# Optimization experiments

Hardware: AMD Instinct MI355X
Metric: run time of the kernel (lower is better)

## Reference

```python
import jax, jax.numpy as jnp
import numpy as np

N_NODES = 50000
N_EDGES = 400000
IN_DIM = 256
EPS_BN = 1e-5


def _bn(x, gamma, beta):
    # BatchNorm over nodes (training-mode batch statistics)
    m = jnp.mean(x, axis=0)
    v = jnp.var(x, axis=0)
    return (x - m) * jax.lax.rsqrt(v + EPS_BN) * gamma + beta


def _gcn(x, W, b, src, dst, n):
    # PyG GCNConv: add self-loops, symmetric deg^-1/2 normalization
    h = x @ W  # [N, F_out]
    deg = jax.ops.segment_sum(jnp.ones_like(dst, dtype=h.dtype), dst, num_segments=n) + 1.0
    dinv = jax.lax.rsqrt(deg)
    coef = dinv[src] * dinv[dst]  # [E]
    agg = jax.ops.segment_sum(h[src] * coef[:, None], dst, num_segments=n)
    agg = agg + h * (dinv * dinv)[:, None]  # self-loop contribution
    return agg + b


def _gat(x, W, a_src, a_dst, b, src, dst, n):
    # PyG GATConv, heads=H, concat=False (mean over heads)
    H, F = a_src.shape
    h = (x @ W).reshape(n, H, F)
    asc = jnp.einsum('nhf,hf->nh', h, a_src)
    adc = jnp.einsum('nhf,hf->nh', h, a_dst)
    loops = jnp.arange(n, dtype=src.dtype)
    s = jnp.concatenate([src, loops])
    d = jnp.concatenate([dst, loops])
    e = jax.nn.leaky_relu(asc[s] + adc[d], 0.2)  # [E+N, H]
    mx = jax.ops.segment_max(e, d, num_segments=n)
    ee = jnp.exp(e - mx[d])
    denom = jax.ops.segment_sum(ee, d, num_segments=n)
    alpha = ee / (denom[d] + 1e-16)  # edge softmax over incoming edges
    out = jax.ops.segment_sum(alpha[:, :, None] * h[s], d, num_segments=n)  # [N,H,F]
    return out.mean(axis=1) + b


def setup_inputs() -> dict:
    key = jax.random.key(0)
    ks = jax.random.split(key, 24)

    def glorot(k, shape):
        fan = shape[0] + shape[-1]
        return jax.random.normal(k, shape, jnp.float32) * np.sqrt(2.0 / fan)

    d = {}
    d['x'] = jax.random.normal(ks[0], (N_NODES, IN_DIM), jnp.float32)
    d['edge_index'] = jax.random.randint(ks[1], (2, N_EDGES), 0, N_NODES, jnp.int32)
    # GCNConv 1: 256 -> 256
    d['w1'] = glorot(ks[2], (IN_DIM, 256)); d['b1'] = jnp.zeros((256,), jnp.float32)
    d['g1'] = jnp.ones((256,), jnp.float32); d['be1'] = jnp.zeros((256,), jnp.float32)
    # GATConv: 256 -> 128, heads=4, concat=False
    d['gat_w'] = glorot(ks[3], (256, 4 * 128))
    d['gat_as'] = glorot(ks[4], (4, 128))
    d['gat_ad'] = glorot(ks[5], (4, 128))
    d['gat_b'] = jnp.zeros((128,), jnp.float32)
    d['g2'] = jnp.ones((128,), jnp.float32); d['be2'] = jnp.zeros((128,), jnp.float32)
    # GCNConv 3..5
    d['w3'] = glorot(ks[6], (128, 64)); d['b3'] = jnp.zeros((64,), jnp.float32)
    d['g3'] = jnp.ones((64,), jnp.float32); d['be3'] = jnp.zeros((64,), jnp.float32)
    d['w4'] = glorot(ks[7], (64, 32)); d['b4'] = jnp.zeros((32,), jnp.float32)
    d['g4'] = jnp.ones((32,), jnp.float32); d['be4'] = jnp.zeros((32,), jnp.float32)
    d['w5'] = glorot(ks[8], (32, 16)); d['b5'] = jnp.zeros((16,), jnp.float32)
    d['g5'] = jnp.ones((16,), jnp.float32); d['be5'] = jnp.zeros((16,), jnp.float32)
    # FC head
    d['fw1'] = glorot(ks[9], (16, 8)); d['fb1'] = jnp.zeros((8,), jnp.float32)
    d['fw2'] = glorot(ks[10], (8, 3)); d['fb2'] = jnp.zeros((3,), jnp.float32)
    return d


def reference(x, edge_index, w1, b1, g1, be1, gat_w, gat_as, gat_ad, gat_b, g2, be2,
              w3, b3, g3, be3, w4, b4, g4, be4, w5, b5, g5, be5, fw1, fb1, fw2, fb2):
    n = x.shape[0]
    src, dst = edge_index[0], edge_index[1]
    lrelu = lambda h: jax.nn.leaky_relu(h, 0.01)
    # dropout is identity in eval mode
    h = lrelu(_bn(_gcn(x, w1, b1, src, dst, n), g1, be1))
    h = lrelu(_bn(_gat(h, gat_w, gat_as, gat_ad, gat_b, src, dst, n), g2, be2))
    h = lrelu(_bn(_gcn(h, w3, b3, src, dst, n), g3, be3))
    h = lrelu(_bn(_gcn(h, w4, b4, src, dst, n), g4, be4))
    h = lrelu(_bn(_gcn(h, w5, b5, src, dst, n), g5, be5))
    h = lrelu(h @ fw1 + fb1)
    h = h @ fw2 + fb2
    return jax.nn.log_softmax(h, axis=1)
```

## Files before the change

kernel.cpp:

```cpp
#include <hip/hip_runtime.h>

#define NN 50000
#define NE 400000
#define GSTAT 2048

typedef short bf16x8 __attribute__((ext_vector_type(8)));
typedef float f32x4 __attribute__((ext_vector_type(4)));

__device__ __forceinline__ float lrelu01(float v) { return v >= 0.f ? v : 0.01f * v; }
__device__ __forceinline__ float lrelu02(float v) { return v >= 0.f ? v : 0.2f * v; }

__device__ __forceinline__ ushort f2bf(float f) {
  union { float f; unsigned u; } v; v.f = f;
  unsigned u = v.u;
  return (ushort)((u + 0x7FFFu + ((u >> 16) & 1u)) >> 16);
}
__device__ __forceinline__ float bf2f(ushort u) {
  union { unsigned u; float f; } v; v.u = ((unsigned)u) << 16;
  return v.f;
}

__global__ void wprep(const float* __restrict__ w1, const float* __restrict__ gw,
                      const float* __restrict__ w3, const float* __restrict__ w4,
                      const float* __restrict__ w5,
                      ushort* __restrict__ w1T, ushort* __restrict__ gwT,
                      ushort* __restrict__ w3T, ushort* __restrict__ w4T,
                      ushort* __restrict__ w5T) {
  int i = blockIdx.x * 256 + threadIdx.x;
  const float* W; ushort* WT; int K, N, j;
  if (i < 65536)        { W = w1; WT = w1T; K = 256; N = 256; j = i; }
  else if (i < 196608)  { W = gw; WT = gwT; K = 256; N = 512; j = i - 65536; }
  else if (i < 204800)  { W = w3; WT = w3T; K = 128; N = 64;  j = i - 196608; }
  else if (i < 206848)  { W = w4; WT = w4T; K = 64;  N = 32;  j = i - 204800; }
  else if (i < 207360)  { W = w5; WT = w5T; K = 32;  N = 16;  j = i - 206848; }
  else return;
  int k = j / N, c = j % N;
  WT[(size_t)c * K + k] = f2bf(W[(size_t)j]);
}

__global__ void count_kernel(const int* __restrict__ dst, int* __restrict__ counts, int e) {
  int i = blockIdx.x * 256 + threadIdx.x;
  if (i < e) atomicAdd(&counts[dst[i]], 1);
}

__global__ __launch_bounds__(256) void block_count_sum(const int* __restrict__ counts,
                                                       int* __restrict__ bsum,
                                                       float* __restrict__ dinv, int n) {
  int i = blockIdx.x * 256 + threadIdx.x;
  int c = (i < n) ? counts[i] : 0;
  if (i < n) dinv[i] = rsqrtf((float)c + 1.0f);
  int s = c;
#pragma unroll
  for (int off = 32; off > 0; off >>= 1) s += __shfl_down(s, off);
  __shared__ int ws[4];
  if ((threadIdx.x & 63) == 0) ws[threadIdx.x >> 6] = s;
  __syncthreads();
  if (threadIdx.x == 0) bsum[blockIdx.x] = ws[0] + ws[1] + ws[2] + ws[3];
}

__global__ __launch_bounds__(256) void scan_bsum(int* __restrict__ bsum, int nb) {
  __shared__ int sh[256];
  int v = (threadIdx.x < nb) ? bsum[threadIdx.x] : 0;
  sh[threadIdx.x] = v;
  __syncthreads();
  for (int off = 1; off < 256; off <<= 1) {
    int t = (threadIdx.x >= off) ? sh[threadIdx.x - off] : 0;
    __syncthreads();
    sh[threadIdx.x] += t;
    __syncthreads();
  }
  if (threadIdx.x < nb) bsum[threadIdx.x] = sh[threadIdx.x] - v;
}

__global__ __launch_bounds__(256) void row_start_kernel(const int* __restrict__ counts,
                                                        const int* __restrict__ bsum,
                                                        int* __restrict__ row_start, int n) {
  __shared__ int sh[256];
  int i = blockIdx.x * 256 + threadIdx.x;
  int c = (i < n) ? counts[i] : 0;
  sh[threadIdx.x] = c;
  __syncthreads();
  for (int off = 1; off < 256; off <<= 1) {
    int t = (threadIdx.x >= off) ? sh[threadIdx.x - off] : 0;
    __syncthreads();
    sh[threadIdx.x] += t;
    __syncthreads();
  }
  int incl = sh[threadIdx.x];
  int base = bsum[blockIdx.x];
  if (i < n) row_start[i] = base + incl - c;
  if (i == n - 1) row_start[n] = base + incl;
}

__global__ void fill_kernel(const int* __restrict__ src, const int* __restrict__ dst,
                            const int* __restrict__ row_start, int* __restrict__ cursor,
                            int* __restrict__ csr, int e) {
  int i = blockIdx.x * 256 + threadIdx.x;
  if (i >= e) return;
  int d = dst[i];
  int pos = atomicAdd(&cursor[d], 1);
  csr[row_start[d] + pos] = src[i];
}

__global__ __launch_bounds__(256) void gemm_mfma_x(const float* __restrict__ A,
                                                   const ushort* __restrict__ BT,
                                                   ushort* __restrict__ C,
                                                   int M, int K, int N,
                                                   const float* __restrict__ rowscale) {
  __shared__ ushort As[128][40];
  __shared__ ushort Bs[128][40];
  const int tid = threadIdx.x;
  const int bm = blockIdx.x * 128;
  const int bn = blockIdx.y * 128;
  const int wave = tid >> 6, lane = tid & 63;
  const int wr = (wave >> 1) * 64;
  const int wc = (wave & 1) * 64;
  const int lr = lane & 15;
  const int lk = (lane >> 4) * 8;

  f32x4 acc[4][4];
#pragma unroll
  for (int m = 0; m < 4; ++m)
#pragma unroll
    for (int n = 0; n < 4; ++n)
#pragma unroll
      for (int q = 0; q < 4; ++q) acc[m][n][q] = 0.f;

  for (int k0 = 0; k0 < K; k0 += 32) {
#pragma unroll
    for (int it = 0; it < 2; ++it) {
      int s = tid + it * 256;
      int r = s >> 2;
      int c = (s & 3) * 8;
      int grow = bm + r; if (grow >= M) grow = M - 1;
      float4 va = *reinterpret_cast<const float4*>(&A[(size_t)grow * K + k0 + c]);
      float4 vb = *reinterpret_cast<const float4*>(&A[(size_t)grow * K + k0 + c + 4]);
      ushort4 lo = make_ushort4(f2bf(va.x), f2bf(va.y), f2bf(va.z), f2bf(va.w));
      ushort4 hi = make_ushort4(f2bf(vb.x), f2bf(vb.y), f2bf(vb.z), f2bf(vb.w));
      *reinterpret_cast<ushort4*>(&As[r][c]) = lo;
      *reinterpret_cast<ushort4*>(&As[r][c + 4]) = hi;
    }
#pragma unroll
    for (int it = 0; it < 2; ++it) {
      int s = tid + it * 256;
      int r = s >> 2;
      int c = (s & 3) * 8;
      int4 v = *reinterpret_cast<const int4*>(&BT[(size_t)(bn + r) * K + k0 + c]);
      *reinterpret_cast<int4*>(&Bs[r][c]) = v;
    }
    __syncthreads();

    bf16x8 af[4], bfr[4];
#pragma unroll
    for (int m = 0; m < 4; ++m)
      af[m] = *reinterpret_cast<const bf16x8*>(&As[wr + m * 16 + lr][lk]);
#pragma unroll
    for (int n = 0; n < 4; ++n)
      bfr[n] = *reinterpret_cast<const bf16x8*>(&Bs[wc + n * 16 + lr][lk]);
#pragma unroll
    for (int m = 0; m < 4; ++m)
#pragma unroll
      for (int n = 0; n < 4; ++n)
        acc[m][n] = __builtin_amdgcn_mfma_f32_16x16x32_bf16(af[m], bfr[n], acc[m][n], 0, 0, 0);
    __syncthreads();
  }

  const int rbase = (lane >> 4) * 4;
  const int cbase = lane & 15;
#pragma unroll
  for (int m = 0; m < 4; ++m) {
#pragma unroll
    for (int q = 0; q < 4; ++q) {
      int row = bm + wr + m * 16 + rbase + q;
      if (row >= M) continue;
      float sc = rowscale ? rowscale[row] : 1.f;
#pragma unroll
      for (int n = 0; n < 4; ++n) {
        int col = bn + wc + n * 16 + cbase;
        C[(size_t)row * N + col] = f2bf(acc[m][n][q] * sc);
      }
    }
  }
}

__global__ __launch_bounds__(256) void gemm_mfma_bn(const ushort* __restrict__ A,
                                                    const ushort* __restrict__ BT,
                                                    ushort* __restrict__ C,
                                                    int M, int K, int N,
                                                    const float* __restrict__ rowscale,
                                                    const float* __restrict__ stats,
                                                    const float* __restrict__ gamma,
                                                    const float* __restrict__ beta) {
  __shared__ ushort As[128][40];
  __shared__ ushort Bs[128][40];
  __shared__ float scl[256], shl[256];
  const int tid = threadIdx.x;
  const float inv_n = 1.0f / (float)NN;
  for (int k = tid; k < K; k += 256) {
    float mean = stats[k] * inv_n;
    float var = stats[K + k] * inv_n - mean * mean;
    float sc = gamma[k] * rsqrtf(var + 1e-5f);
    scl[k] = sc;
    shl[k] = beta[k] - mean * sc;
  }
  const int bm = blockIdx.x * 128;
  const int bn = blockIdx.y * 128;
  const int wave = tid >> 6, lane = tid & 63;
  const int wr = (wave >> 1) * 64;
  const int wc = (wave & 1) * 64;
  const int lr = lane & 15;
  const int lk = (lane >> 4) * 8;

  f32x4 acc[4][4];
#pragma unroll
  for (int m = 0; m < 4; ++m)
#pragma unroll
    for (int n = 0; n < 4; ++n)
#pragma unroll
      for (int q = 0; q < 4; ++q) acc[m][n][q] = 0.f;
  __syncthreads();

  for (int k0 = 0; k0 < K; k0 += 32) {
#pragma unroll
    for (int it = 0; it < 2; ++it) {
      int s = tid + it * 256;
      int r = s >> 2;
      int c = (s & 3) * 8;
      int grow = bm + r; if (grow >= M) grow = M - 1;
      int4 v = *reinterpret_cast<const int4*>(&A[(size_t)grow * K + k0 + c]);
      ushort* u = reinterpret_cast<ushort*>(&v);
      ushort tmp[8];
#pragma unroll
      for (int j = 0; j < 8; ++j) {
        float f = bf2f(u[j]) * scl[k0 + c + j] + shl[k0 + c + j];
        tmp[j] = f2bf(f >= 0.f ? f : 0.01f * f);
      }
      *reinterpret_cast<int4*>(&As[r][c]) = *reinterpret_cast<int4*>(tmp);
    }
#pragma unroll
    for (int it = 0; it < 2; ++it) {
      int s = tid + it * 256;
      int r = s >> 2;
      int c = (s & 3) * 8;
      int4 v = *reinterpret_cast<const int4*>(&BT[(size_t)(bn + r) * K + k0 + c]);
      *reinterpret_cast<int4*>(&Bs[r][c]) = v;
    }
    __syncthreads();

    bf16x8 af[4], bfr[4];
#pragma unroll
    for (int m = 0; m < 4; ++m)
      af[m] = *reinterpret_cast<const bf16x8*>(&As[wr + m * 16 + lr][lk]);
#pragma unroll
    for (int n = 0; n < 4; ++n)
      bfr[n] = *reinterpret_cast<const bf16x8*>(&Bs[wc + n * 16 + lr][lk]);
#pragma unroll
    for (int m = 0; m < 4; ++m)
#pragma unroll
      for (int n = 0; n < 4; ++n)
        acc[m][n] = __builtin_amdgcn_mfma_f32_16x16x32_bf16(af[m], bfr[n], acc[m][n], 0, 0, 0);
    __syncthreads();
  }

  const int rbase = (lane >> 4) * 4;
  const int cbase = lane & 15;
#pragma unroll
  for (int m = 0; m < 4; ++m) {
#pragma unroll
    for (int q = 0; q < 4; ++q) {
      int row = bm + wr + m * 16 + rbase + q;
      if (row >= M) continue;
      float sc = rowscale ? rowscale[row] : 1.f;
#pragma unroll
      for (int n = 0; n < 4; ++n) {
        int col = bn + wc + n * 16 + cbase;
        C[(size_t)row * N + col] = f2bf(acc[m][n][q] * sc);
      }
    }
  }
}

template <int TN>
__global__ __launch_bounds__(256) void gemm_mfma_n_bn(const ushort* __restrict__ A,
                                                      const ushort* __restrict__ BT,
                                                      ushort* __restrict__ C,
                                                      int M, int K,
                                                      const float* __restrict__ rowscale,
                                                      const float* __restrict__ stats,
                                                      const float* __restrict__ gamma,
                                                      const float* __restrict__ beta) {
  __shared__ ushort As[128][40];
  __shared__ ushort Bs[TN][40];
  __shared__ float scl[128], shl[128];
  const int tid = threadIdx.x;
  const float inv_n = 1.0f / (float)NN;
  if (tid < K) {
    float mean = stats[tid] * inv_n;
    float var = stats[K + tid] * inv_n - mean * mean;
    float sc = gamma[tid] * rsqrtf(var + 1e-5f);
    scl[tid] = sc;
    shl[tid] = beta[tid] - mean * sc;
  }
  const int bm = blockIdx.x * 128;
  const int wave = tid >> 6, lane = tid & 63;
  const int wr = wave * 32;
  const int lr = lane & 15;
  const int lk = (lane >> 4) * 8;
  constexpr int NF = TN / 16;

  f32x4 acc[2][NF];
#pragma unroll
  for (int m = 0; m < 2; ++m)
#pragma unroll
    for (int n = 0; n < NF; ++n)
#pragma unroll
      for (int q = 0; q < 4; ++q) acc[m][n][q] = 0.f;
  __syncthreads();

  for (int k0 = 0; k0 < K; k0 += 32) {
#pragma unroll
    for (int it = 0; it < 2; ++it) {
      int s = tid + it * 256;
      int r = s >> 2;
      int c = (s & 3) * 8;
      int grow = bm + r; if (grow >= M) grow = M - 1;
      int4 v = *reinterpret_cast<const int4*>(&A[(size_t)grow * K + k0 + c]);
      ushort* u = reinterpret_cast<ushort*>(&v);
      ushort tmp[8];
#pragma unroll
      for (int j = 0; j < 8; ++j) {
        float f = bf2f(u[j]) * scl[k0 + c + j] + shl[k0 + c + j];
        tmp[j] = f2bf(f >= 0.f ? f : 0.01f * f);
      }
      *reinterpret_cast<int4*>(&As[r][c]) = *reinterpret_cast<int4*>(tmp);
    }
    if (tid < TN * 4) {
      int r = tid >> 2;
      int c = (tid & 3) * 8;
      int4 v = *reinterpret_cast<const int4*>(&BT[(size_t)r * K + k0 + c]);
      *reinterpret_cast<int4*>(&Bs[r][c]) = v;
    }
    __syncthreads();

    bf16x8 af[2], bfr[NF];
#pragma unroll
    for (int m = 0; m < 2; ++m)
      af[m] = *reinterpret_cast<const bf16x8*>(&As[wr + m * 16 + lr][lk]);
#pragma unroll
    for (int n = 0; n < NF; ++n)
      bfr[n] = *reinterpret_cast<const bf16x8*>(&Bs[n * 16 + lr][lk]);
#pragma unroll
    for (int m = 0; m < 2; ++m)
#pragma unroll
      for (int n = 0; n < NF; ++n)
        acc[m][n] = __builtin_amdgcn_mfma_f32_16x16x32_bf16(af[m], bfr[n], acc[m][n], 0, 0, 0);
    __syncthreads();
  }

  const int rbase = (lane >> 4) * 4;
  const int cbase = lane & 15;
#pragma unroll
  for (int m = 0; m < 2; ++m) {
#pragma unroll
    for (int q = 0; q < 4; ++q) {
      int row = bm + wr + m * 16 + rbase + q;
      if (row >= M) continue;
      float sc = rowscale ? rowscale[row] : 1.f;
#pragma unroll
      for (int n = 0; n < NF; ++n) {
        int col = n * 16 + cbase;
        C[(size_t)row * TN + col] = f2bf(acc[m][n][q] * sc);
      }
    }
  }
}

template <int F>
__global__ __launch_bounds__(256) void gcn_agg_stats(const ushort* __restrict__ h,
                                                     const int* __restrict__ row_start,
                                                     const int* __restrict__ csr,
                                                     const float* __restrict__ dinv,
                                                     ushort* __restrict__ out,
                                                     float* __restrict__ partials, int n) {
  constexpr int LPN = F / 8;
  constexpr int NPB = 256 / LPN;
  const int tid = threadIdx.x;
  const int sub = tid / LPN;
  const int f8 = (tid % LPN) * 8;
  float ps[8], pq[8];
#pragma unroll
  for (int j = 0; j < 8; ++j) { ps[j] = 0.f; pq[j] = 0.f; }

  for (int node = blockIdx.x * NPB + sub; node < n; node += GSTAT * NPB) {
    float di = dinv[node];
    float a[8];
    {
      int4 v = *reinterpret_cast<const int4*>(&h[(size_t)node * F + f8]);
      const ushort* u = reinterpret_cast<const ushort*>(&v);
#pragma unroll
      for (int j = 0; j < 8; ++j) a[j] = bf2f(u[j]);
    }
    int s0 = row_start[node], s1 = row_start[node + 1];
    int e = s0;
    for (; e + 3 < s1; e += 4) {
      int sA = csr[e], sB = csr[e + 1], sC = csr[e + 2], sD = csr[e + 3];
      int4 vA = *reinterpret_cast<const int4*>(&h[(size_t)sA * F + f8]);
      int4 vB = *reinterpret_cast<const int4*>(&h[(size_t)sB * F + f8]);
      int4 vC = *reinterpret_cast<const int4*>(&h[(size_t)sC * F + f8]);
      int4 vD = *reinterpret_cast<const int4*>(&h[(size_t)sD * F + f8]);
      const ushort* uA = reinterpret_cast<const ushort*>(&vA);
      const ushort* uB = reinterpret_cast<const ushort*>(&vB);
      const ushort* uC = reinterpret_cast<const ushort*>(&vC);
      const ushort* uD = reinterpret_cast<const ushort*>(&vD);
#pragma unroll
      for (int j = 0; j < 8; ++j)
        a[j] += (bf2f(uA[j]) + bf2f(uB[j])) + (bf2f(uC[j]) + bf2f(uD[j]));
    }
    for (; e < s1; ++e) {
      int sA = csr[e];
      int4 vA = *reinterpret_cast<const int4*>(&h[(size_t)sA * F + f8]);
      const ushort* uA = reinterpret_cast<const ushort*>(&vA);
#pragma unroll
      for (int j = 0; j < 8; ++j) a[j] += bf2f(uA[j]);
    }
    ushort u[8];
#pragma unroll
    for (int j = 0; j < 8; ++j) {
      a[j] *= di;
      u[j] = f2bf(a[j]);
      ps[j] += a[j];
      pq[j] += a[j] * a[j];
    }
    *reinterpret_cast<int4*>(&out[(size_t)node * F + f8]) = *reinterpret_cast<int4*>(u);
  }

  __shared__ float red[NPB][2 * F];
#pragma unroll
  for (int j = 0; j < 8; ++j) {
    red[sub][f8 + j] = ps[j];
    red[sub][F + f8 + j] = pq[j];
  }
  __syncthreads();
  for (int c = tid; c < 2 * F; c += 256) {
    float t = 0.f;
#pragma unroll 4
    for (int s = 0; s < NPB; ++s) t += red[s][c];
    partials[(size_t)c * GSTAT + blockIdx.x] = t;
  }
}

__global__ __launch_bounds__(256) void gat_agg_fused(const ushort* __restrict__ hg,
                                                     const int* __restrict__ row_start,
                                                     const int* __restrict__ csr,
                                                     const float* __restrict__ asc,
                                                     const float* __restrict__ adc,
                                                     ushort* __restrict__ out,
                                                     float* __restrict__ partials, int n) {
  const int tid = threadIdx.x;
  const int wave = tid >> 6, lane = tid & 63;
  const int h = lane >> 4;
  const int l = lane & 15;
  const int f8 = l * 8;
  float ps[8], pq[8];
#pragma unroll
  for (int j = 0; j < 8; ++j) { ps[j] = 0.f; pq[j] = 0.f; }

  for (int node = blockIdx.x * 4 + wave; node < n; node += GSTAT * 4) {
    float ad = adc[node * 4 + h];
    float es = lrelu02(asc[node * 4 + h] + ad);
    int s0 = row_start[node], s1 = row_start[node + 1];
    float m = es;
    for (int e = s0 + l; e < s1; e += 16)
      m = fmaxf(m, lrelu02(asc[csr[e] * 4 + h] + ad));
#pragma unroll
    for (int off = 1; off < 16; off <<= 1) m = fmaxf(m, __shfl_xor(m, off));
    float wself = __expf(es - m);
    float d = (l == 0) ? wself : 0.f;
    for (int e = s0 + l; e < s1; e += 16)
      d += __expf(lrelu02(asc[csr[e] * 4 + h] + ad) - m);
#pragma unroll
    for (int off = 1; off < 16; off <<= 1) d += __shfl_xor(d, off);
    float coef = 0.25f / (d + 1e-16f);
    const ushort* base = hg + h * 128 + f8;
    float a[8];
    {
      int4 v = *reinterpret_cast<const int4*>(base + (size_t)node * 512);
      const ushort* u = reinterpret_cast<const ushort*>(&v);
#pragma unroll
      for (int j = 0; j < 8; ++j) a[j] = wself * bf2f(u[j]);
    }
    int e = s0;
    for (; e + 1 < s1; e += 2) {
      int sA = csr[e], sB = csr[e + 1];
      float wA = __expf(lrelu02(asc[sA * 4 + h] + ad) - m);
      float wB = __expf(lrelu02(asc[sB * 4 + h] + ad) - m);
      int4 vA = *reinterpret_cast<const int4*>(base + (size_t)sA * 512);
      int4 vB = *reinterpret_cast<const int4*>(base + (size_t)sB * 512);
      const ushort* uA = reinterpret_cast<const ushort*>(&vA);
      const ushort* uB = reinterpret_cast<const ushort*>(&vB);
#pragma unroll
      for (int j = 0; j < 8; ++j) a[j] += wA * bf2f(uA[j]) + wB * bf2f(uB[j]);
    }
    if (e < s1) {
      int sA = csr[e];
      float wA = __expf(lrelu02(asc[sA * 4 + h] + ad) - m);
      int4 vA = *reinterpret_cast<const int4*>(base + (size_t)sA * 512);
      const ushort* uA = reinterpret_cast<const ushort*>(&vA);
#pragma unroll
      for (int j = 0; j < 8; ++j) a[j] += wA * bf2f(uA[j]);
    }
#pragma unroll
    for (int j = 0; j < 8; ++j) {
      a[j] *= coef;
      a[j] += __shfl_xor(a[j], 16);
      a[j] += __shfl_xor(a[j], 32);
    }
    if (h == 0) {
      ushort u[8];
#pragma unroll
      for (int j = 0; j < 8; ++j) {
        u[j] = f2bf(a[j]);
        ps[j] += a[j];
        pq[j] += a[j] * a[j];
      }
      *reinterpret_cast<int4*>(&out[(size_t)node * 128 + f8]) = *reinterpret_cast<int4*>(u);
    }
  }

  __shared__ float red[4][256];
  if (h == 0) {
#pragma unroll
    for (int j = 0; j < 8; ++j) {
      red[wave][f8 + j] = ps[j];
      red[wave][128 + f8 + j] = pq[j];
    }
  }
  __syncthreads();
  if (tid < 256) {
    int c = tid;
    float t = red[0][c] + red[1][c] + red[2][c] + red[3][c];
    partials[(size_t)c * GSTAT + blockIdx.x] = t;
  }
}

__global__ __launch_bounds__(256) void bn_reduce_col(const float* __restrict__ partials,
                                                     float* __restrict__ stats) {
  int c = blockIdx.x;
  float s = 0.f;
  for (int b = threadIdx.x; b < GSTAT; b += 256) s += partials[(size_t)c * GSTAT + b];
#pragma unroll
  for (int off = 32; off > 0; off >>= 1) s += __shfl_down(s, off);
  __shared__ float ws[4];
  if ((threadIdx.x & 63) == 0) ws[threadIdx.x >> 6] = s;
  __syncthreads();
  if (threadIdx.x == 0) stats[c] = ws[0] + ws[1] + ws[2] + ws[3];
}

__global__ __launch_bounds__(256) void gat_scores_bf(const ushort* __restrict__ hg,
                                                     const float* __restrict__ a_src,
                                                     const float* __restrict__ a_dst,
                                                     float* __restrict__ asc,
                                                     float* __restrict__ adc, int n) {
  int node = blockIdx.x;
  int head = threadIdx.x >> 6;
  int lane = threadIdx.x & 63;
  ushort2 v = *reinterpret_cast<const ushort2*>(&hg[(size_t)node * 512 + head * 128 + lane * 2]);
  float v0 = bf2f(v.x), v1 = bf2f(v.y);
  float s = v0 * a_src[head * 128 + lane * 2] + v1 * a_src[head * 128 + lane * 2 + 1];
  float d = v0 * a_dst[head * 128 + lane * 2] + v1 * a_dst[head * 128 + lane * 2 + 1];
#pragma unroll
  for (int off = 32; off > 0; off >>= 1) {
    s += __shfl_down(s, off);
    d += __shfl_down(d, off);
  }
  if (lane == 0) {
    asc[node * 4 + head] = s;
    adc[node * 4 + head] = d;
  }
}

__global__ __launch_bounds__(256) void head_kernel_bn(const ushort* __restrict__ h,
                                                      const float* __restrict__ stats,
                                                      const float* __restrict__ g5,
                                                      const float* __restrict__ be5,
                                                      const float* __restrict__ fw1,
                                                      const float* __restrict__ fb1,
                                                      const float* __restrict__ fw2,
                                                      const float* __restrict__ fb2,
                                                      float* __restrict__ out, int n) {
  __shared__ float scl[16], shl[16];
  if (threadIdx.x < 16) {
    const float inv_n = 1.0f / (float)NN;
    int k = threadIdx.x;
    float mean = stats[k] * inv_n;
    float var = stats[16 + k] * inv_n - mean * mean;
    float sc = g5[k] * rsqrtf(var + 1e-5f);
    scl[k] = sc;
    shl[k] = be5[k] - mean * sc;
  }
  __syncthreads();
  int i = blockIdx.x * 256 + threadIdx.x;
  if (i >= n) return;
  int4 ra = *reinterpret_cast<const int4*>(&h[(size_t)i * 16]);
  int4 rb = *reinterpret_cast<const int4*>(&h[(size_t)i * 16 + 8]);
  ushort u[16];
  *reinterpret_cast<int4*>(&u[0]) = ra;
  *reinterpret_cast<int4*>(&u[8]) = rb;
  float xr[16];
#pragma unroll
  for (int k = 0; k < 16; ++k) {
    float v = bf2f(u[k]) * scl[k] + shl[k];
    xr[k] = v >= 0.f ? v : 0.01f * v;
  }
  float z[8];
#pragma unroll
  for (int j = 0; j < 8; ++j) z[j] = fb1[j];
#pragma unroll
  for (int k = 0; k < 16; ++k) {
    float a = xr[k];
#pragma unroll
    for (int j = 0; j < 8; ++j) z[j] += a * fw1[k * 8 + j];
  }
#pragma unroll
  for (int j = 0; j < 8; ++j) z[j] = lrelu01(z[j]);
  float l[3];
#pragma unroll
  for (int j = 0; j < 3; ++j) l[j] = fb2[j];
#pragma unroll
  for (int k = 0; k < 8; ++k) {
    float a = z[k];
#pragma unroll
    for (int j = 0; j < 3; ++j) l[j] += a * fw2[k * 3 + j];
  }
  float mx = fmaxf(l[0], fmaxf(l[1], l[2]));
  float se = __expf(l[0] - mx) + __expf(l[1] - mx) + __expf(l[2] - mx);
  float ls = __logf(se);
#pragma unroll
  for (int j = 0; j < 3; ++j) out[(size_t)i * 3 + j] = l[j] - mx - ls;
}

extern "C" void kernel_launch(void* const* d_in, const int* in_sizes, int n_in,
                              void* d_out, int out_size, void* d_ws, size_t ws_size,
                              hipStream_t stream) {
  const float* x      = (const float*)d_in[0];
  const int*   ei     = (const int*)d_in[1];
  const int*   srcI   = ei;
  const int*   dstI   = ei + NE;
  const float* w1     = (const float*)d_in[2];
  const float* g1     = (const float*)d_in[4];
  const float* be1    = (const float*)d_in[5];
  const float* gat_w  = (const float*)d_in[6];
  const float* gat_as = (const float*)d_in[7];
  const float* gat_ad = (const float*)d_in[8];
  const float* g2     = (const float*)d_in[10];
  const float* be2    = (const float*)d_in[11];
  const float* w3     = (const float*)d_in[12];
  const float* g3     = (const float*)d_in[14];
  const float* be3    = (const float*)d_in[15];
  const float* w4     = (const float*)d_in[16];
  const float* g4     = (const float*)d_in[18];
  const float* be4    = (const float*)d_in[19];
  const float* w5     = (const float*)d_in[20];
  const float* g5     = (const float*)d_in[22];
  const float* be5    = (const float*)d_in[23];
  const float* fw1    = (const float*)d_in[24];
  const float* fb1    = (const float*)d_in[25];
  const float* fw2    = (const float*)d_in[26];
  const float* fb2    = (const float*)d_in[27];
  float* out = (float*)d_out;

  char* wsp = (char*)d_ws;
  size_t off = 0;
  auto alloc = [&](size_t bytes) -> void* {
    void* p = wsp + off;
    off += (bytes + 255) & ~(size_t)255;
    return p;
  };
  ushort* hw_bf  = (ushort*)alloc((size_t)NN * 512 * 2);
  ushort* r1     = (ushort*)alloc((size_t)NN * 256 * 2);
  ushort* r2     = (ushort*)alloc((size_t)NN * 128 * 2);
  ushort* r3     = (ushort*)alloc((size_t)NN * 64 * 2);
  ushort* r4     = (ushort*)alloc((size_t)NN * 32 * 2);
  ushort* r5     = (ushort*)alloc((size_t)NN * 16 * 2);
  ushort* w1T    = (ushort*)alloc((size_t)256 * 256 * 2);
  ushort* gwT    = (ushort*)alloc((size_t)512 * 256 * 2);
  ushort* w3T    = (ushort*)alloc((size_t)64 * 128 * 2);
  ushort* w4T    = (ushort*)alloc((size_t)32 * 64 * 2);
  ushort* w5T    = (ushort*)alloc((size_t)16 * 32 * 2);
  float*  dinv   = (float*)alloc((size_t)NN * 4);
  int*    counts = (int*)alloc((size_t)NN * 4);
  int*    cursor = (int*)alloc((size_t)NN * 4);
  int*    rstart = (int*)alloc((size_t)(NN + 4) * 4);
  int*    bsum   = (int*)alloc((size_t)256 * 4);
  int*    csr    = (int*)alloc((size_t)NE * 4);
  float*  asc    = (float*)alloc((size_t)NN * 4 * 4);
  float*  adc    = (float*)alloc((size_t)NN * 4 * 4);
  float*  stats  = (float*)alloc(2048);
  float*  partials = (float*)alloc((size_t)512 * GSTAT * 4);

  const int egrid = (NE + 255) / 256;
  const int ngrid = (NN + 255) / 256;
  const int mblocks = (NN + 127) / 128;

  hipMemsetAsync(counts, 0, (size_t)NN * 4, stream);
  hipMemsetAsync(cursor, 0, (size_t)NN * 4, stream);
  count_kernel<<<egrid, 256, 0, stream>>>(dstI, counts, NE);
  block_count_sum<<<ngrid, 256, 0, stream>>>(counts, bsum, dinv, NN);
  scan_bsum<<<1, 256, 0, stream>>>(bsum, ngrid);
  row_start_kernel<<<ngrid, 256, 0, stream>>>(counts, bsum, rstart, NN);
  fill_kernel<<<egrid, 256, 0, stream>>>(srcI, dstI, rstart, cursor, csr, NE);

  wprep<<<810, 256, 0, stream>>>(w1, gat_w, w3, w4, w5, w1T, gwT, w3T, w4T, w5T);

  gemm_mfma_x<<<dim3(mblocks, 2), 256, 0, stream>>>(x, w1T, hw_bf, NN, 256, 256, dinv);
  gcn_agg_stats<256><<<GSTAT, 256, 0, stream>>>(hw_bf, rstart, csr, dinv, r1, partials, NN);
  bn_reduce_col<<<512, 256, 0, stream>>>(partials, stats);

  gemm_mfma_bn<<<dim3(mblocks, 4), 256, 0, stream>>>(r1, gwT, hw_bf, NN, 256, 512, nullptr,
                                                     stats, g1, be1);
  gat_scores_bf<<<NN, 256, 0, stream>>>(hw_bf, gat_as, gat_ad, asc, adc, NN);
  gat_agg_fused<<<GSTAT, 256, 0, stream>>>(hw_bf, rstart, csr, asc, adc, r2, partials, NN);
  bn_reduce_col<<<256, 256, 0, stream>>>(partials, stats);

  gemm_mfma_n_bn<64><<<mblocks, 256, 0, stream>>>(r2, w3T, hw_bf, NN, 128, dinv, stats, g2, be2);
  gcn_agg_stats<64><<<GSTAT, 256, 0, stream>>>(hw_bf, rstart, csr, dinv, r3, partials, NN);
  bn_reduce_col<<<128, 256, 0, stream>>>(partials, stats);

  gemm_mfma_n_bn<32><<<mblocks, 256, 0, stream>>>(r3, w4T, hw_bf, NN, 64, dinv, stats, g3, be3);
  gcn_agg_stats<32><<<GSTAT, 256, 0, stream>>>(hw_bf, rstart, csr, dinv, r4, partials, NN);
  bn_reduce_col<<<64, 256, 0, stream>>>(partials, stats);

  gemm_mfma_n_bn<16><<<mblocks, 256, 0, stream>>>(r4, w5T, hw_bf, NN, 32, dinv, stats, g4, be4);
  gcn_agg_stats<16><<<GSTAT, 256, 0, stream>>>(hw_bf, rstart, csr, dinv, r5, partials, NN);
  bn_reduce_col<<<32, 256, 0, stream>>>(partials, stats);

  head_kernel_bn<<<ngrid, 256, 0, stream>>>(r5, stats, g5, be5, fw1, fb1, fw2, fb2, out, NN);
}
```

Before: 388.0 us.

## Split GAT edge softmax into separate kernel producing normalized attention weights

Moves the per-node edge-softmax (max, exp, denominator, normalization) out of the GAT aggregation kernel into a new kernel that writes per-edge normalized alpha and a self-loop weight. The aggregation kernel then reads those precomputed weights instead of recomputing the exponential three times per edge inside the wide gather loop. In exchange it adds a kernel launch plus an extra alpha buffer written and read through global memory, and the softmax kernel runs one thread per (node, head) with serial edge loops and strided accesses.

```diff
diff --git a/kernel.cpp b/kernel.cpp
--- a/kernel.cpp
+++ b/kernel.cpp
@@ -449,13 +449,43 @@
   }
 }
 
-__global__ __launch_bounds__(256) void gat_agg_fused(const ushort* __restrict__ hg,
-                                                     const int* __restrict__ row_start,
-                                                     const int* __restrict__ csr,
-                                                     const float* __restrict__ asc,
-                                                     const float* __restrict__ adc,
-                                                     ushort* __restrict__ out,
-                                                     float* __restrict__ partials, int n) {
+__global__ __launch_bounds__(256) void gat_softmax_norm(const int* __restrict__ row_start,
+                                                        const int* __restrict__ csr,
+                                                        const float* __restrict__ asc,
+                                                        const float* __restrict__ adc,
+                                                        float* __restrict__ alpha,
+                                                        float* __restrict__ wnorm, int n) {
+  int i = blockIdx.x * 256 + threadIdx.x;
+  if (i >= 4 * n) return;
+  int node = i >> 2, h = i & 3;
+  int s0 = row_start[node], s1 = row_start[node + 1];
+  float ad = adc[i];
+  float eself = lrelu02(asc[i] + ad);
+  float m = eself;
+  for (int e = s0; e < s1; ++e) {
+    float v = lrelu02(asc[csr[e] * 4 + h] + ad);
+    alpha[(size_t)e * 4 + h] = v;
+    m = fmaxf(m, v);
+  }
+  float ws = __expf(eself - m);
+  float den = ws;
+  for (int e = s0; e < s1; ++e) {
+    float w = __expf(alpha[(size_t)e * 4 + h] - m);
+    alpha[(size_t)e * 4 + h] = w;
+    den += w;
+  }
+  float coef = 0.25f / (den + 1e-16f);
+  wnorm[i] = ws * coef;
+  for (int e = s0; e < s1; ++e) alpha[(size_t)e * 4 + h] *= coef;
+}
+
+__global__ __launch_bounds__(256) void gat_agg_v2(const ushort* __restrict__ hg,
+                                                  const int* __restrict__ row_start,
+                                                  const int* __restrict__ csr,
+                                                  const float* __restrict__ alpha,
+                                                  const float* __restrict__ wnorm,
+                                                  ushort* __restrict__ out,
+                                                  float* __restrict__ partials, int n) {
   const int tid = threadIdx.x;
   const int wave = tid >> 6, lane = tid & 63;
   const int h = lane >> 4;
@@ -465,35 +495,22 @@
 #pragma unroll
   for (int j = 0; j < 8; ++j) { ps[j] = 0.f; pq[j] = 0.f; }
 
+  const ushort* base = hg + h * 128 + f8;
   for (int node = blockIdx.x * 4 + wave; node < n; node += GSTAT * 4) {
-    float ad = adc[node * 4 + h];
-    float es = lrelu02(asc[node * 4 + h] + ad);
-    int s0 = row_start[node], s1 = row_start[node + 1];
-    float m = es;
-    for (int e = s0 + l; e < s1; e += 16)
-      m = fmaxf(m, lrelu02(asc[csr[e] * 4 + h] + ad));
-#pragma unroll
-    for (int off = 1; off < 16; off <<= 1) m = fmaxf(m, __shfl_xor(m, off));
-    float wself = __expf(es - m);
-    float d = (l == 0) ? wself : 0.f;
-    for (int e = s0 + l; e < s1; e += 16)
-      d += __expf(lrelu02(asc[csr[e] * 4 + h] + ad) - m);
-#pragma unroll
-    for (int off = 1; off < 16; off <<= 1) d += __shfl_xor(d, off);
-    float coef = 0.25f / (d + 1e-16f);
-    const ushort* base = hg + h * 128 + f8;
     float a[8];
     {
+      float w = wnorm[node * 4 + h];
       int4 v = *reinterpret_cast<const int4*>(base + (size_t)node * 512);
       const ushort* u = reinterpret_cast<const ushort*>(&v);
 #pragma unroll
-      for (int j = 0; j < 8; ++j) a[j] = wself * bf2f(u[j]);
-    }
+      for (int j = 0; j < 8; ++j) a[j] = w * bf2f(u[j]);
+    }
+    int s0 = row_start[node], s1 = row_start[node + 1];
     int e = s0;
     for (; e + 1 < s1; e += 2) {
       int sA = csr[e], sB = csr[e + 1];
-      float wA = __expf(lrelu02(asc[sA * 4 + h] + ad) - m);
-      float wB = __expf(lrelu02(asc[sB * 4 + h] + ad) - m);
+      float wA = alpha[(size_t)e * 4 + h];
+      float wB = alpha[(size_t)(e + 1) * 4 + h];
       int4 vA = *reinterpret_cast<const int4*>(base + (size_t)sA * 512);
       int4 vB = *reinterpret_cast<const int4*>(base + (size_t)sB * 512);
       const ushort* uA = reinterpret_cast<const ushort*>(&vA);
@@ -503,7 +520,7 @@
     }
     if (e < s1) {
       int sA = csr[e];
-      float wA = __expf(lrelu02(asc[sA * 4 + h] + ad) - m);
+      float wA = alpha[(size_t)e * 4 + h];
       int4 vA = *reinterpret_cast<const int4*>(base + (size_t)sA * 512);
       const ushort* uA = reinterpret_cast<const ushort*>(&vA);
 #pragma unroll
@@ -511,7 +528,6 @@
     }
 #pragma unroll
     for (int j = 0; j < 8; ++j) {
-      a[j] *= coef;
       a[j] += __shfl_xor(a[j], 16);
       a[j] += __shfl_xor(a[j], 32);
     }
@@ -536,7 +552,7 @@
     }
   }
   __syncthreads();
-  if (tid < 256) {
+  {
     int c = tid;
     float t = red[0][c] + red[1][c] + red[2][c] + red[3][c];
     partials[(size_t)c * GSTAT + blockIdx.x] = t;
@@ -695,6 +711,8 @@
   int*    csr    = (int*)alloc((size_t)NE * 4);
   float*  asc    = (float*)alloc((size_t)NN * 4 * 4);
   float*  adc    = (float*)alloc((size_t)NN * 4 * 4);
+  float*  wnorm  = (float*)alloc((size_t)NN * 4 * 4);
+  float*  alpha  = (float*)alloc((size_t)NE * 4 * 4);
   float*  stats  = (float*)alloc(2048);
   float*  partials = (float*)alloc((size_t)512 * GSTAT * 4);
 
@@ -719,7 +737,8 @@
   gemm_mfma_bn<<<dim3(mblocks, 4), 256, 0, stream>>>(r1, gwT, hw_bf, NN, 256, 512, nullptr,
                                                      stats, g1, be1);
   gat_scores_bf<<<NN, 256, 0, stream>>>(hw_bf, gat_as, gat_ad, asc, adc, NN);
-  gat_agg_fused<<<GSTAT, 256, 0, stream>>>(hw_bf, rstart, csr, asc, adc, r2, partials, NN);
+  gat_softmax_norm<<<(4 * NN + 255) / 256, 256, 0, stream>>>(rstart, csr, asc, adc, alpha, wnorm, NN);
+  gat_agg_v2<<<GSTAT, 256, 0, stream>>>(hw_bf, rstart, csr, alpha, wnorm, r2, partials, NN);
   bn_reduce_col<<<256, 256, 0, stream>>>(partials, stats);
 
   gemm_mfma_n_bn<64><<<mblocks, 256, 0, stream>>>(r2, w3T, hw_bf, NN, 128, dinv, stats, g2, be2);
```

Measured after the change: 397.7 us. +2.5%, slower.
